# Performance work log

Measured on AMD Instinct MI355X. Metric: run time of the kernel, lower is better.

## Reference

```python
import jax, jax.numpy as jnp
import numpy as np

B, QL, D = 4, 1024, 1024
H, HD = 16, 64
KVL = 2048


def setup_inputs() -> dict:
    key = jax.random.key(0)
    ks = jax.random.split(key, 6)
    scale = 1.0 / np.sqrt(D)
    return {
        "hidden_states": jax.random.normal(ks[0], (B, QL, D), dtype=jnp.float32),
        "key_states": jax.random.normal(ks[1], (B, H, KVL, HD), dtype=jnp.float32),
        "value_states": jax.random.normal(ks[2], (B, H, KVL, HD), dtype=jnp.float32),
        "attention_mask": jnp.zeros((B, 1, 1, KVL), dtype=jnp.float32),
        "Wq": jax.random.normal(ks[3], (D, D), dtype=jnp.float32) * scale,
        "Wo": jax.random.normal(ks[4], (D, D), dtype=jnp.float32) * scale,
    }


def reference(hidden_states, key_states, value_states, attention_mask, Wq, Wo):
    batch = hidden_states.shape[0]
    # Q projection (T5 Linear has no bias), split heads: [B, H, Q, HD]
    q = jnp.einsum("bqd,de->bqe", hidden_states, Wq)
    q = q.reshape(batch, -1, H, HD).transpose(0, 2, 1, 3)
    # NOTE: T5 attention has NO 1/sqrt(d) scaling
    scores = jnp.einsum("bhqd,bhkd->bhqk", q, key_states) + attention_mask
    attn = jax.nn.softmax(scores.astype(jnp.float32), axis=-1).astype(scores.dtype)
    out = jnp.einsum("bhqk,bhkd->bhqd", attn, value_states)
    out = out.transpose(0, 2, 1, 3).reshape(batch, -1, H * HD)
    return jnp.einsum("bqe,ed->bqd", out, Wo)
```

## Files before the change

kernel.cpp:

```cpp
#include <hip/hip_runtime.h>
#include <hip/hip_bf16.h>
#include <hip/hip_fp16.h>
#include <stdint.h>

typedef _Float16 f16;
typedef _Float16 f16x2 __attribute__((ext_vector_type(2)));
typedef _Float16 f16x4 __attribute__((ext_vector_type(4)));
typedef _Float16 f16x8 __attribute__((ext_vector_type(8)));
typedef float f32x4 __attribute__((ext_vector_type(4)));
typedef float f32x16 __attribute__((ext_vector_type(16)));
typedef uint32_t u32x4 __attribute__((ext_vector_type(4)));

#define B_ 4
#define QL_ 1024
#define D_ 1024
#define H_ 16
#define HD_ 64
#define KVL_ 2048
#define L2E 1.44269504088896f

__device__ __forceinline__ void g2lds16(const void* g, void* l) {
    __builtin_amdgcn_global_load_lds(
        (const __attribute__((address_space(1))) uint32_t*)g,
        (__attribute__((address_space(3))) uint32_t*)l,
        16, 0, 0);
}

union U8 { uint32_t u[4]; f16x8 v; };

__device__ __forceinline__ uint32_t pkrtz(float a, float b) {
    auto t = __builtin_amdgcn_cvt_pkrtz(a, b);
    return __builtin_bit_cast(uint32_t, t);
}

__global__ void prep_wq(const float* __restrict__ Wq, f16* __restrict__ Wq_t) {
    __shared__ float t[64][65];
    int b2 = blockIdx.x, tid = threadIdx.x;
    int k0 = (b2 >> 4) << 6, n0 = (b2 & 15) << 6;
    int rr = tid >> 4, c4 = (tid & 15) << 2;
#pragma unroll
    for (int i = 0; i < 4; ++i) {
        int r = i * 16 + rr;
        float4 v = *(const float4*)(Wq + (size_t)(k0 + r) * 1024 + n0 + c4);
        t[r][c4 + 0] = v.x; t[r][c4 + 1] = v.y; t[r][c4 + 2] = v.z; t[r][c4 + 3] = v.w;
    }
    __syncthreads();
#pragma unroll
    for (int i = 0; i < 4; ++i) {
        int n = i * 16 + rr;
        f16x4 o;
#pragma unroll
        for (int j = 0; j < 4; ++j) o[j] = (f16)t[c4 + j][n];
        *(f16x4*)(Wq_t + (size_t)(n0 + n) * 1024 + k0 + c4) = o;
    }
}

__global__ __launch_bounds__(512) void gemm0_fused(
    const float* __restrict__ hs, const f16* __restrict__ BT, f16* __restrict__ q_h,
    const float* __restrict__ K, f16* __restrict__ K_h,
    const float* __restrict__ V, f16* __restrict__ V_t,
    const float* __restrict__ Wo, f16* __restrict__ Wo_t,
    const float* __restrict__ mask, f16* __restrict__ em16) {
    __shared__ char shmem[49152];
    int bid = blockIdx.x, tid = threadIdx.x;

    if (bid < 512) {
        char* Alds = shmem;
        char* Blds = shmem + 32768;
        int xcd = bid & 7, sx = bid >> 3;
        int bm = xcd * 4 + (sx & 3);
        int bn = sx >> 2;
        int w = tid >> 6, l = tid & 63;
        int l15 = l & 15, lg = l >> 4;
        int wm = w >> 1, wn = w & 1;
        f32x4 acc[2][2] = {};

        int rA0 = tid >> 3, c80 = tid & 7, cc0 = c80 ^ (rA0 & 7);
        const float* ags0 = hs + ((size_t)(bm * 128 + rA0) * 1024 + cc0 * 8);
        const float* ags1 = ags0 + 65536;
        int aw0 = rA0 * 128 + c80 * 16;
        int aw1 = aw0 + 8192;

        int rB = w * 8 + (l >> 3);
        int ccB = (l & 7) ^ (rB & 7);
        const char* bgp = (const char*)BT + ((size_t)(bn * 64 + rB) * 1024 + ccB * 8) * 2;
        int boB = w * 1024;

        int aoff[2][2], boff[2][2];
#pragma unroll
        for (int ks = 0; ks < 2; ++ks)
#pragma unroll
            for (int m = 0; m < 2; ++m) {
                int ra = wm * 32 + m * 16 + l15;
                aoff[ks][m] = ra * 128 + ((ks * 64 + lg * 16) ^ ((ra & 7) << 4));
                int rb = wn * 32 + m * 16 + l15;
                boff[ks][m] = rb * 128 + ((ks * 64 + lg * 16) ^ ((rb & 7) << 4));
            }

        f32x4 a0, a1, a2, a3;
#define ALOAD(buf, o32, oB)                                    \
    {                                                          \
        a0 = *(const f32x4*)(ags0 + (o32));                    \
        a1 = *(const f32x4*)(ags0 + (o32) + 4);                \
        a2 = *(const f32x4*)(ags1 + (o32));                    \
        a3 = *(const f32x4*)(ags1 + (o32) + 4);                \
        g2lds16(bgp + (oB), Blds + (buf) * 8192 + boB);        \
    }
#define CVTW(buf)                                                              \
    {                                                                          \
        asm volatile("s_waitcnt vmcnt(1)" ::: "memory");                       \
        u32x4 w0 = { pkrtz(a0[0], a0[1]), pkrtz(a0[2], a0[3]),                 \
                     pkrtz(a1[0], a1[1]), pkrtz(a1[2], a1[3]) };               \
        *(u32x4*)(Alds + (buf) * 16384 + aw0) = w0;                            \
        u32x4 w1 = { pkrtz(a2[0], a2[1]), pkrtz(a2[2], a2[3]),                 \
                     pkrtz(a3[0], a3[1]), pkrtz(a3[2], a3[3]) };               \
        *(u32x4*)(Alds + (buf) * 16384 + aw1) = w1;                            \
    }
#define GCOMP(buf)                                                               \
    _Pragma("unroll") for (int ks = 0; ks < 2; ++ks) {                           \
        f16x8 af[2], bf[2];                                                      \
        af[0] = *(const f16x8*)(Alds + (buf) * 16384 + aoff[ks][0]);             \
        af[1] = *(const f16x8*)(Alds + (buf) * 16384 + aoff[ks][1]);             \
        bf[0] = *(const f16x8*)(Blds + (buf) * 8192 + boff[ks][0]);              \
        bf[1] = *(const f16x8*)(Blds + (buf) * 8192 + boff[ks][1]);              \
        _Pragma("unroll") for (int m = 0; m < 2; ++m)                            \
            _Pragma("unroll") for (int n = 0; n < 2; ++n)                        \
                acc[m][n] = __builtin_amdgcn_mfma_f32_16x16x32_f16(af[m], bf[n], acc[m][n], 0, 0, 0); \
    }
#define SYNCV()                                                          \
    {                                                                    \
        asm volatile("s_waitcnt vmcnt(0) lgkmcnt(0)" ::: "memory");      \
        __syncthreads();                                                 \
    }

        ALOAD(0, 0, 0);
        CVTW(0);
        SYNCV();
        for (int t2 = 0; t2 < 8; ++t2) {
            ALOAD(1, 64, 128);
            GCOMP(0);
            CVTW(1);
            SYNCV();
            if (t2 < 7) ALOAD(0, 128, 256);
            GCOMP(1);
            if (t2 < 7) CVTW(0);
            SYNCV();
            ags0 += 128; ags1 += 128; bgp += 256;
        }
#pragma unroll
        for (int m = 0; m < 2; ++m)
#pragma unroll
            for (int n = 0; n < 2; ++n)
#pragma unroll
                for (int i = 0; i < 4; ++i) {
                    int row = bm * 128 + wm * 32 + m * 16 + lg * 4 + i;
                    int col = bn * 64 + wn * 32 + n * 16 + l15;
                    float v = acc[m][n][i] * L2E;
                    int b = row >> 10, q = row & 1023, h = col >> 6, d = col & 63;
                    q_h[(((size_t)b * H_ + h) * QL_ + q) * HD_ + d] = (f16)v;
                }
#undef ALOAD
#undef CVTW
#undef GCOMP
#undef SYNCV
    } else if (bid < 1536) {
        int t0 = (bid - 512) * 512 + tid;
#pragma unroll
        for (int rep = 0; rep < 2; ++rep) {
            int U = t0 + rep * 524288;
            int bh = U >> 14, rem = U & 16383;
            int ch = rem >> 9, r2 = rem & 511;
            int dsl = r2 >> 7, r3 = r2 & 127;
            int kv = r3 >> 1, hi2 = r3 & 1;
            const float* sp = K + (((size_t)bh * KVL_ + ch * 64 + kv) * HD_ + dsl * 16 + hi2 * 8);
            f16x8 o;
#pragma unroll
            for (int j = 0; j < 8; ++j) o[j] = (f16)sp[j];
            *(f16x8*)(K_h + (size_t)U * 8) = o;
        }
    } else if (bid < 2560) {
        int sub = tid >> 8, st2 = tid & 255;
        int vb = (bid - 1536) * 2 + sub;
        int bh = vb >> 5, ch = vb & 31;
        int b = bh >> 4;
        float (*tt)[65] = (float(*)[65])(shmem + sub * 16640);
        float* emv = (float*)(shmem + 33280 + sub * 256);
        int rr = st2 >> 4, c4 = (st2 & 15) << 2;
#pragma unroll
        for (int i = 0; i < 4; ++i) {
            int r = i * 16 + rr;
            float4 v = *(const float4*)(V + ((size_t)bh * KVL_ + ch * 64 + r) * HD_ + c4);
            tt[r][c4 + 0] = v.x; tt[r][c4 + 1] = v.y; tt[r][c4 + 2] = v.z; tt[r][c4 + 3] = v.w;
        }
        if (st2 < 64)
            emv[st2] = __builtin_amdgcn_exp2f(mask[(size_t)b * KVL_ + ch * 64 + st2] * L2E);
        __syncthreads();
#pragma unroll
        for (int rep = 0; rep < 2; ++rep) {
            int u = st2 + rep * 256;
            int st = u >> 7, d = (u >> 1) & 63, hi2 = u & 1;
            f16x8 o;
#pragma unroll
            for (int j = 0; j < 8; ++j) {
                int kvl = st * 16 + (j & 3) + 8 * (j >> 2) + 4 * hi2;
                o[j] = (f16)(tt[kvl][d] * emv[kvl]);
            }
            *(f16x8*)(V_t + ((size_t)(bh * 32 + ch) * 512 + u) * 8) = o;
        }
        if (((bh & 15) == 0) && st2 < 64) {
            int kb = st2 >> 5, hi2v = (st2 >> 4) & 1, slot = st2 & 15;
            int kvv = kb * 32 + (slot & 3) + 8 * (slot >> 2) + 4 * hi2v;
            em16[(((size_t)b * 64 + ch * 2 + kb) * 2 + hi2v) * 16 + slot] = (f16)emv[kvv];
        }
    } else {
        int sub = tid >> 8, st2 = tid & 255;
        int b2 = (bid - 2560) * 2 + sub;
        float (*tt)[65] = (float(*)[65])(shmem + sub * 16640);
        int k0 = (b2 >> 4) << 6, n0 = (b2 & 15) << 6;
        int rr = st2 >> 4, c4 = (st2 & 15) << 2;
#pragma unroll
        for (int i = 0; i < 4; ++i) {
            int r = i * 16 + rr;
            float4 v = *(const float4*)(Wo + (size_t)(k0 + r) * 1024 + n0 + c4);
            tt[r][c4 + 0] = v.x; tt[r][c4 + 1] = v.y; tt[r][c4 + 2] = v.z; tt[r][c4 + 3] = v.w;
        }
        __syncthreads();
#pragma unroll
        for (int i = 0; i < 4; ++i) {
            int n = i * 16 + rr;
            f16x4 o;
#pragma unroll
            for (int j = 0; j < 4; ++j) o[j] = (f16)tt[c4 + j][n];
            *(f16x4*)(Wo_t + (size_t)(n0 + n) * 1024 + k0 + c4) = o;
        }
    }
}

__global__ __launch_bounds__(512) void gemm_tn1(
    const f16* __restrict__ A, const f16* __restrict__ BT, float* __restrict__ Cout) {
    __shared__ char Alds[2][16384];
    __shared__ char Blds[2][8192];
    int d0 = blockIdx.x;
    int xcd = d0 & 7, sx = d0 >> 3;
    int bm = xcd * 4 + (sx & 3);
    int bn = sx >> 2;
    int tid = threadIdx.x, w = tid >> 6, l = tid & 63;
    int l15 = l & 15, lg = l >> 4;
    int wm = w >> 1, wn = w & 1;
    f32x4 acc[2][2] = {};

    const char* ag0; const char* ag1; int ao0, ao1;
    {
        int i0 = w, i1 = w + 8;
        int r0 = i0 * 8 + (l >> 3), r1 = i1 * 8 + (l >> 3);
        int c0 = (l & 7) ^ (r0 & 7), c1 = (l & 7) ^ (r1 & 7);
        ag0 = (const char*)A + ((size_t)(bm * 128 + r0) * 1024 + c0 * 8) * 2;
        ag1 = (const char*)A + ((size_t)(bm * 128 + r1) * 1024 + c1 * 8) * 2;
        ao0 = i0 * 1024; ao1 = i1 * 1024;
    }
    int rB = w * 8 + (l >> 3);
    int ccB = (l & 7) ^ (rB & 7);
    const char* bgp = (const char*)BT + ((size_t)(bn * 64 + rB) * 1024 + ccB * 8) * 2;
    int boB = w * 1024;

    int aoff[2][2], boff[2][2];
#pragma unroll
    for (int ks = 0; ks < 2; ++ks)
#pragma unroll
        for (int m = 0; m < 2; ++m) {
            int ra = wm * 32 + m * 16 + l15;
            aoff[ks][m] = ra * 128 + ((ks * 64 + lg * 16) ^ ((ra & 7) << 4));
            int rb = wn * 32 + m * 16 + l15;
            boff[ks][m] = rb * 128 + ((ks * 64 + lg * 16) ^ ((rb & 7) << 4));
        }
    const char* Ab = &Alds[0][0];
    const char* Bb = &Blds[0][0];

#define GSTAGE(buf, soff)                                      \
    {                                                          \
        g2lds16(ag0 + (soff), &Alds[buf][ao0]);                \
        g2lds16(ag1 + (soff), &Alds[buf][ao1]);                \
        g2lds16(bgp + (soff), &Blds[buf][boB]);                \
    }
#define GCOMP(buf)                                                               \
    _Pragma("unroll") for (int ks = 0; ks < 2; ++ks) {                           \
        f16x8 af[2], bf[2];                                                      \
        af[0] = *(const f16x8*)(Ab + (buf) * 16384 + aoff[ks][0]);               \
        af[1] = *(const f16x8*)(Ab + (buf) * 16384 + aoff[ks][1]);               \
        bf[0] = *(const f16x8*)(Bb + (buf) * 8192 + boff[ks][0]);                \
        bf[1] = *(const f16x8*)(Bb + (buf) * 8192 + boff[ks][1]);                \
        _Pragma("unroll") for (int m = 0; m < 2; ++m)                            \
            _Pragma("unroll") for (int n = 0; n < 2; ++n)                        \
                acc[m][n] = __builtin_amdgcn_mfma_f32_16x16x32_f16(af[m], bf[n], acc[m][n], 0, 0, 0); \
    }

    GSTAGE(0, 0);
    asm volatile("s_waitcnt vmcnt(0)" ::: "memory");
    __syncthreads();
    for (int t2 = 0; t2 < 8; ++t2) {
        GSTAGE(1, 128);
        GCOMP(0);
        asm volatile("s_waitcnt vmcnt(0)" ::: "memory");
        __syncthreads();
        if (t2 < 7) GSTAGE(0, 256);
        GCOMP(1);
        asm volatile("s_waitcnt vmcnt(0)" ::: "memory");
        __syncthreads();
        ag0 += 256; ag1 += 256; bgp += 256;
    }
#pragma unroll
    for (int m = 0; m < 2; ++m)
#pragma unroll
        for (int n = 0; n < 2; ++n)
#pragma unroll
            for (int i = 0; i < 4; ++i) {
                int row = bm * 128 + wm * 32 + m * 16 + lg * 4 + i;
                int col = bn * 64 + wn * 32 + n * 16 + l15;
                Cout[(size_t)row * 1024 + col] = acc[m][n][i];
            }
#undef GSTAGE
#undef GCOMP
}

__global__ __launch_bounds__(256, 4) void attn_fused(
    const f16* __restrict__ qh, const f16* __restrict__ kh, const f16* __restrict__ vt,
    const f16* __restrict__ em16, f16* __restrict__ aout) {
    __shared__ char lds_buf[36864];
    __shared__ float frl[4][32];

    int tid = threadIdx.x, w = tid >> 6, l = tid & 63;
    int l31 = l & 31, hi = l >> 5;
    int d0 = blockIdx.x;
    int xcd = d0 & 7, sx = d0 >> 3;
    int bh = xcd * 8 + (sx & 7);
    int qt = sx >> 3;
    int b = bh >> 4, h = bh & 15;

    const char* lbase = lds_buf + l31 * 32 + hi * 16;
    const char* embase = lds_buf + 32768 + hi * 32;

    f16x8 Qf[4];
    {
        const f16* qp = qh + ((size_t)bh * QL_ + qt * 128 + w * 32 + l31) * HD_ + hi * 8;
#pragma unroll
        for (int ds_ = 0; ds_ < 4; ++ds_) Qf[ds_] = *(const f16x8*)(qp + ds_ * 16);
    }

    const char* kgp0 = (const char*)kh + ((size_t)(bh * 32) * 512 + w * 2 * 64 + l) * 16;
    const char* kgp1 = kgp0 + 1024;
    const char* vgp0 = (const char*)vt + ((size_t)(bh * 32) * 512 + w * 2 * 64 + l) * 16;
    const char* vgp1 = vgp0 + 1024;
    char* kl0 = lds_buf + w * 2048;
    char* kl1 = kl0 + 1024;
    char* vl0 = lds_buf + 16384 + w * 2048;
    char* vl1 = vl0 + 1024;

#define PREF(buf, soff)                                  \
    {                                                    \
        g2lds16(kgp0 + (soff), kl0 + (buf) * 8192);      \
        g2lds16(kgp1 + (soff), kl1 + (buf) * 8192);      \
        g2lds16(vgp0 + (soff), vl0 + (buf) * 8192);      \
        g2lds16(vgp1 + (soff), vl1 + (buf) * 8192);      \
    }

    float mrun = -1e30f, ssA = 0.f, ssB = 0.f;
    f32x16 acc[2] = {};
    int emoff = 0;

#define BODY(buf, kb, emo)                                                                \
    {                                                                                     \
        f32x16 St = {};                                                                   \
        __builtin_amdgcn_s_setprio(1);                                                    \
        _Pragma("unroll") for (int ds_ = 0; ds_ < 4; ++ds_) {                             \
            f16x8 kf = *(const f16x8*)(lbase + (buf) * 8192 + ds_ * 2048 + (kb) * 1024);  \
            St = __builtin_amdgcn_mfma_f32_32x32x16_f16(kf, Qf[ds_], St, 0, 0, 0);        \
        }                                                                                 \
        __builtin_amdgcn_s_setprio(0);                                                    \
        float a0 = fmaxf(fmaxf(St[0], St[1]), St[2]);                                     \
        float a1 = fmaxf(fmaxf(St[3], St[4]), St[5]);                                     \
        float a2 = fmaxf(fmaxf(St[6], St[7]), St[8]);                                     \
        float a3 = fmaxf(fmaxf(St[9], St[10]), St[11]);                                   \
        float a4 = fmaxf(fmaxf(St[12], St[13]), St[14]);                                  \
        float lmax = fmaxf(fmaxf(fmaxf(a0, a1), St[15]), fmaxf(a2, fmaxf(a3, a4)));       \
        if (__any(lmax > mrun + 12.f)) {                                                  \
            float pm = fmaxf(lmax, __shfl_xor(lmax, 32));                                 \
            float mn = fmaxf(mrun, pm);                                                   \
            float fac = __builtin_amdgcn_exp2f(mrun - mn);                                \
            mrun = mn; ssA *= fac; ssB *= fac;                                            \
            frl[w][l31] = fac;                                                            \
            asm volatile("s_waitcnt lgkmcnt(0)" ::: "memory");                            \
            _Pragma("unroll") for (int g4 = 0; g4 < 4; ++g4) {                            \
                f32x4 fv = *(const f32x4*)&frl[w][g4 * 8 + hi * 4];                       \
                _Pragma("unroll") for (int c = 0; c < 2; ++c)                             \
                    _Pragma("unroll") for (int j = 0; j < 4; ++j)                         \
                        acc[c][g4 * 4 + j] *= fv[j];                                      \
            }                                                                             \
        }                                                                                 \
        uint32_t pk[8];                                                                   \
        _Pragma("unroll") for (int i = 0; i < 8; ++i) {                                   \
            float p0 = __builtin_amdgcn_exp2f(St[2 * i] - mrun);                          \
            float p1 = __builtin_amdgcn_exp2f(St[2 * i + 1] - mrun);                      \
            pk[i] = pkrtz(p0, p1);                                                        \
        }                                                                                 \
        U8 ea, eb;                                                                        \
        ea.v = *(const f16x8*)(embase + (emo));                                           \
        eb.v = *(const f16x8*)(embase + (emo) + 16);                                      \
        _Pragma("unroll") for (int i = 0; i < 4; ++i) {                                   \
            ssA = __builtin_amdgcn_fdot2(__builtin_bit_cast(f16x2, pk[2 * i]),            \
                                         __builtin_bit_cast(f16x2, (2 * i) < 4 ? ea.u[2 * i] : eb.u[2 * i - 4]), ssA, false); \
            ssB = __builtin_amdgcn_fdot2(__builtin_bit_cast(f16x2, pk[2 * i + 1]),        \
                                         __builtin_bit_cast(f16x2, (2 * i + 1) < 4 ? ea.u[2 * i + 1] : eb.u[2 * i - 3]), ssB, false); \
        }                                                                                 \
        __builtin_amdgcn_s_setprio(1);                                                    \
        _Pragma("unroll") for (int sti = 0; sti < 2; ++sti) {                             \
            U8 pa;                                                                        \
            pa.u[0] = pk[sti * 4 + 0]; pa.u[1] = pk[sti * 4 + 1];                         \
            pa.u[2] = pk[sti * 4 + 2]; pa.u[3] = pk[sti * 4 + 3];                         \
            const int st_ = (kb) * 2 + sti;                                               \
            _Pragma("unroll") for (int c = 0; c < 2; ++c) {                               \
                U8 vb;                                                                    \
                vb.v = *(const f16x8*)(lbase + 16384 + (buf) * 8192 + st_ * 2048 + c * 1024); \
                acc[c] = __builtin_amdgcn_mfma_f32_32x32x16_f16(pa.v, vb.v, acc[c], 0, 0, 0); \
            }                                                                             \
        }                                                                                 \
        __builtin_amdgcn_s_setprio(0);                                                    \
    }

    g2lds16((const char*)em16 + b * 4096 + w * 1024 + l * 16, lds_buf + 32768 + w * 1024);
    PREF(0, 0);
    asm volatile("s_waitcnt vmcnt(0)" ::: "memory");
    __syncthreads();

    for (int it = 0; it < 16; ++it) {
        PREF(1, 8192);
        BODY(0, 0, emoff);
        BODY(0, 1, emoff + 64);
        asm volatile("s_waitcnt vmcnt(0)" ::: "memory");
        __syncthreads();
        if (it < 15) PREF(0, 16384);
        BODY(1, 0, emoff + 128);
        BODY(1, 1, emoff + 192);
        asm volatile("s_waitcnt vmcnt(0)" ::: "memory");
        __syncthreads();
        kgp0 += 16384; kgp1 += 16384; vgp0 += 16384; vgp1 += 16384;
        emoff += 256;
    }

    float ssum = ssA + ssB;
    ssum += __shfl_xor(ssum, 32);
    float rinv = 1.0f / ssum;
    frl[w][l31] = rinv;
    asm volatile("s_waitcnt lgkmcnt(0)" ::: "memory");
#pragma unroll
    for (int g4 = 0; g4 < 4; ++g4) {
        f32x4 rv = *(const f32x4*)&frl[w][g4 * 8 + hi * 4];
#pragma unroll
        for (int c = 0; c < 2; ++c)
#pragma unroll
            for (int j = 0; j < 4; ++j) {
                float o = acc[c][g4 * 4 + j] * rv[j];
                int q = qt * 128 + w * 32 + g4 * 8 + hi * 4 + j;
                int dd = c * 32 + l31;
                aout[((size_t)b * QL_ + q) * D_ + h * HD_ + dd] = (f16)o;
            }
    }
#undef PREF
#undef BODY
}

extern "C" void kernel_launch(void* const* d_in, const int* in_sizes, int n_in,
                              void* d_out, int out_size, void* d_ws, size_t ws_size,
                              hipStream_t stream) {
    const float* hs = (const float*)d_in[0];
    const float* K  = (const float*)d_in[1];
    const float* V  = (const float*)d_in[2];
    const float* mask = (const float*)d_in[3];
    const float* Wq = (const float*)d_in[4];
    const float* Wo = (const float*)d_in[5];
    float* out = (float*)d_out;
    char* ws = (char*)d_ws;

    f16* Wq_t = (f16*)(ws + 0);
    f16* Wo_t = (f16*)(ws + 2097152);
    f16* K_h  = (f16*)(ws + 4194304);
    f16* V_t  = (f16*)(ws + 20971520);
    f16* q_h  = (f16*)(ws + 37748736);
    f16* a_o  = (f16*)(ws + 46137344);
    f16* em16 = (f16*)(ws + 54525952);

    prep_wq<<<256, 256, 0, stream>>>(Wq, Wq_t);
    gemm0_fused<<<2688, 512, 0, stream>>>(hs, Wq_t, q_h, K, K_h, V, V_t,
                                          Wo, Wo_t, mask, em16);
    attn_fused<<<512, 256, 0, stream>>>(q_h, K_h, V_t, em16, a_o);
    gemm_tn1<<<512, 512, 0, stream>>>(a_o, Wo_t, out);
}
```

Before: 103.6 us.

## Split attention KV range across wave pairs and merge partial softmax in LDS

The attention kernel now processes 64 query rows per block instead of 128, using 1024 blocks. The four waves form two groups, and each group handles half of the KV sequence for two 32-row query sub-tiles. At the end, group 1 writes its partial accumulators and running max/sum to swizzled LDS, and group 0 merges them with rescaling before writing output. The aim is to double block-level parallelism so the GPU's CUs are better filled, at the cost of twice the K/V global traffic per query row and an extra LDS merge step.

```diff
diff --git a/kernel.cpp b/kernel.cpp
--- a/kernel.cpp
+++ b/kernel.cpp
@@ -325,54 +325,55 @@
 __global__ __launch_bounds__(256, 4) void attn_fused(
     const f16* __restrict__ qh, const f16* __restrict__ kh, const f16* __restrict__ vt,
     const f16* __restrict__ em16, f16* __restrict__ aout) {
-    __shared__ char lds_buf[36864];
+    __shared__ char lds_buf[32768];
+    __shared__ char em_lds[4096];
     __shared__ float frl[4][32];
+    __shared__ float fr2[2][2][32];
+    __shared__ float2 msx[2][32];
 
     int tid = threadIdx.x, w = tid >> 6, l = tid & 63;
     int l31 = l & 31, hi = l >> 5;
+    int g = w >> 1, qsub = w & 1;
     int d0 = blockIdx.x;
     int xcd = d0 & 7, sx = d0 >> 3;
     int bh = xcd * 8 + (sx & 7);
     int qt = sx >> 3;
     int b = bh >> 4, h = bh & 15;
 
-    const char* lbase = lds_buf + l31 * 32 + hi * 16;
-    const char* embase = lds_buf + 32768 + hi * 32;
+    const char* kread = lds_buf + g * 16384 + l31 * 32 + hi * 16;
+    const char* vread = lds_buf + g * 16384 + 8192 + l31 * 32 + hi * 16;
+    const char* embase = em_lds + hi * 32;
 
     f16x8 Qf[4];
     {
-        const f16* qp = qh + ((size_t)bh * QL_ + qt * 128 + w * 32 + l31) * HD_ + hi * 8;
+        const f16* qp = qh + ((size_t)bh * QL_ + qt * 64 + qsub * 32 + l31) * HD_ + hi * 8;
 #pragma unroll
         for (int ds_ = 0; ds_ < 4; ++ds_) Qf[ds_] = *(const f16x8*)(qp + ds_ * 16);
     }
 
-    const char* kgp0 = (const char*)kh + ((size_t)(bh * 32) * 512 + w * 2 * 64 + l) * 16;
-    const char* kgp1 = kgp0 + 1024;
-    const char* vgp0 = (const char*)vt + ((size_t)(bh * 32) * 512 + w * 2 * 64 + l) * 16;
-    const char* vgp1 = vgp0 + 1024;
-    char* kl0 = lds_buf + w * 2048;
-    char* kl1 = kl0 + 1024;
-    char* vl0 = lds_buf + 16384 + w * 2048;
-    char* vl1 = vl0 + 1024;
-
-#define PREF(buf, soff)                                  \
-    {                                                    \
-        g2lds16(kgp0 + (soff), kl0 + (buf) * 8192);      \
-        g2lds16(kgp1 + (soff), kl1 + (buf) * 8192);      \
-        g2lds16(vgp0 + (soff), vl0 + (buf) * 8192);      \
-        g2lds16(vgp1 + (soff), vl1 + (buf) * 8192);      \
+    const char* kgp = (const char*)kh + ((size_t)(bh * 32 + g * 16) * 512) * 16 + qsub * 4096 + l * 16;
+    const char* vgp = (const char*)vt + ((size_t)(bh * 32 + g * 16) * 512) * 16 + qsub * 2048 + l * 16;
+    char* klw = lds_buf + g * 16384 + qsub * 2048;
+    char* vlw = lds_buf + g * 16384 + 8192 + qsub * 2048;
+
+#define PREF(buf, ko, vo)                                      \
+    {                                                          \
+        g2lds16(kgp + (ko), klw + (buf) * 4096);               \
+        g2lds16(kgp + (ko) + 2048, klw + (buf) * 4096 + 1024); \
+        g2lds16(vgp + (vo), vlw + (buf) * 4096);               \
+        g2lds16(vgp + (vo) + 1024, vlw + (buf) * 4096 + 1024); \
     }
 
     float mrun = -1e30f, ssA = 0.f, ssB = 0.f;
     f32x16 acc[2] = {};
-    int emoff = 0;
-
-#define BODY(buf, kb, emo)                                                                \
+    int emoff = g * 2048;
+
+#define BODY(buf, emo)                                                                    \
     {                                                                                     \
         f32x16 St = {};                                                                   \
         __builtin_amdgcn_s_setprio(1);                                                    \
         _Pragma("unroll") for (int ds_ = 0; ds_ < 4; ++ds_) {                             \
-            f16x8 kf = *(const f16x8*)(lbase + (buf) * 8192 + ds_ * 2048 + (kb) * 1024);  \
+            f16x8 kf = *(const f16x8*)(kread + (buf) * 4096 + ds_ * 1024);                \
             St = __builtin_amdgcn_mfma_f32_32x32x16_f16(kf, Qf[ds_], St, 0, 0, 0);        \
         }                                                                                 \
         __builtin_amdgcn_s_setprio(0);                                                    \
@@ -416,52 +417,71 @@
             U8 pa;                                                                        \
             pa.u[0] = pk[sti * 4 + 0]; pa.u[1] = pk[sti * 4 + 1];                         \
             pa.u[2] = pk[sti * 4 + 2]; pa.u[3] = pk[sti * 4 + 3];                         \
-            const int st_ = (kb) * 2 + sti;                                               \
             _Pragma("unroll") for (int c = 0; c < 2; ++c) {                               \
                 U8 vb;                                                                    \
-                vb.v = *(const f16x8*)(lbase + 16384 + (buf) * 8192 + st_ * 2048 + c * 1024); \
+                vb.v = *(const f16x8*)(vread + (buf) * 4096 + sti * 2048 + c * 1024);     \
                 acc[c] = __builtin_amdgcn_mfma_f32_32x32x16_f16(pa.v, vb.v, acc[c], 0, 0, 0); \
             }                                                                             \
         }                                                                                 \
         __builtin_amdgcn_s_setprio(0);                                                    \
     }
 
-    g2lds16((const char*)em16 + b * 4096 + w * 1024 + l * 16, lds_buf + 32768 + w * 1024);
-    PREF(0, 0);
+    g2lds16((const char*)em16 + b * 4096 + w * 1024 + l * 16, em_lds + w * 1024);
+    PREF(0, 0, 0);
     asm volatile("s_waitcnt vmcnt(0)" ::: "memory");
     __syncthreads();
 
     for (int it = 0; it < 16; ++it) {
-        PREF(1, 8192);
-        BODY(0, 0, emoff);
-        BODY(0, 1, emoff + 64);
+        PREF(1, 1024, 4096);
+        BODY(0, emoff);
         asm volatile("s_waitcnt vmcnt(0)" ::: "memory");
         __syncthreads();
-        if (it < 15) PREF(0, 16384);
-        BODY(1, 0, emoff + 128);
-        BODY(1, 1, emoff + 192);
+        if (it < 15) PREF(0, 8192, 8192);
+        BODY(1, emoff + 64);
         asm volatile("s_waitcnt vmcnt(0)" ::: "memory");
         __syncthreads();
-        kgp0 += 16384; kgp1 += 16384; vgp0 += 16384; vgp1 += 16384;
-        emoff += 256;
+        kgp += 8192; vgp += 8192; emoff += 128;
     }
 
     float ssum = ssA + ssB;
     ssum += __shfl_xor(ssum, 32);
-    float rinv = 1.0f / ssum;
-    frl[w][l31] = rinv;
-    asm volatile("s_waitcnt lgkmcnt(0)" ::: "memory");
-#pragma unroll
-    for (int g4 = 0; g4 < 4; ++g4) {
-        f32x4 rv = *(const f32x4*)&frl[w][g4 * 8 + hi * 4];
+    char* exch = lds_buf;
+    if (g == 1) {
+        int base = qsub * 8192 + l * 128;
+#pragma unroll
+        for (int i = 0; i < 8; ++i) {
+            int c = i >> 2, j0 = (i & 3) * 4;
+            f32x4 vv = { acc[c][j0], acc[c][j0 + 1], acc[c][j0 + 2], acc[c][j0 + 3] };
+            *(f32x4*)(exch + base + ((i * 16) ^ ((l & 7) << 4))) = vv;
+        }
+        if (hi == 0) msx[qsub][l31] = make_float2(mrun, ssum);
+    }
+    __syncthreads();
+    if (g == 0) {
+        float2 mb = msx[qsub][l31];
+        float m = fmaxf(mrun, mb.x);
+        float fA = __builtin_amdgcn_exp2f(mrun - m);
+        float fB = __builtin_amdgcn_exp2f(mb.x - m);
+        float s = ssum * fA + mb.y * fB;
+        float rinv = 1.0f / s;
+        if (hi == 0) { fr2[qsub][0][l31] = fA * rinv; fr2[qsub][1][l31] = fB * rinv; }
+        asm volatile("s_waitcnt lgkmcnt(0)" ::: "memory");
+        int base = qsub * 8192 + l * 128;
 #pragma unroll
         for (int c = 0; c < 2; ++c)
 #pragma unroll
-            for (int j = 0; j < 4; ++j) {
-                float o = acc[c][g4 * 4 + j] * rv[j];
-                int q = qt * 128 + w * 32 + g4 * 8 + hi * 4 + j;
-                int dd = c * 32 + l31;
-                aout[((size_t)b * QL_ + q) * D_ + h * HD_ + dd] = (f16)o;
+            for (int g4 = 0; g4 < 4; ++g4) {
+                f32x4 gAv = *(const f32x4*)&fr2[qsub][0][g4 * 8 + hi * 4];
+                f32x4 gBv = *(const f32x4*)&fr2[qsub][1][g4 * 8 + hi * 4];
+                int i = c * 4 + g4;
+                f32x4 pv = *(const f32x4*)(exch + base + ((i * 16) ^ ((l & 7) << 4)));
+#pragma unroll
+                for (int j = 0; j < 4; ++j) {
+                    float o = acc[c][g4 * 4 + j] * gAv[j] + pv[j] * gBv[j];
+                    int q = qt * 64 + qsub * 32 + g4 * 8 + hi * 4 + j;
+                    int dd = c * 32 + l31;
+                    aout[((size_t)b * QL_ + q) * D_ + h * HD_ + dd] = (f16)o;
+                }
             }
     }
 #undef PREF
@@ -491,6 +511,6 @@
     prep_wq<<<256, 256, 0, stream>>>(Wq, Wq_t);
     gemm0_fused<<<2688, 512, 0, stream>>>(hs, Wq_t, q_h, K, K_h, V, V_t,
                                           Wo, Wo_t, mask, em16);
-    attn_fused<<<512, 256, 0, stream>>>(q_h, K_h, V_t, em16, a_o);
+    attn_fused<<<1024, 256, 0, stream>>>(q_h, K_h, V_t, em16, a_o);
     gemm_tn1<<<512, 512, 0, stream>>>(a_o, Wo_t, out);
 }
```

Result: slower. 107.3 us (+3.6%).
